# Kernel optimization log

Measured on AMD Instinct MI355X. Metric: run time of the kernel, lower is better.

## Reference

```python
import jax, jax.numpy as jnp
import numpy as np


def setup_inputs() -> dict:
    key = jax.random.key(0)
    k1, k2, k3, k4 = jax.random.split(key, 4)
    B, C, H, W = 4, 48, 512, 512
    T, ws = 3, 64
    # factor matrices (per TensorMultiplication_einsum, T summation terms)
    # init scale: 1/(init_temperature**(1/3) * sqrt(out_dim)) with init_temperature=1.0
    Ws = jax.random.normal(k2, (T, ws, ws), jnp.float32) / np.sqrt(ws)
    Hs = jax.random.normal(k3, (T, ws, ws), jnp.float32) / np.sqrt(ws)
    Cs = jax.random.normal(k4, (T, C, C), jnp.float32) / np.sqrt(C)
    x = jax.random.normal(k1, (B, C, H, W), jnp.float32)
    return {"x": x, "Ws": Ws, "Hs": Hs, "Cs": Cs, "window_size": ws}


def reference(x, Ws, Hs, Cs, window_size):
    """FeatureProcessingBlock forward:
      window_partition -> sum_t einsum('bchw,wW,hH,cC->bCHW') -> window_reverse.
    The window partition/reverse reshapes are fused into one einsum over the
    blocked view (p,q index the window grid; h,w index within-window pixels).
    """
    B, C, H, W = x.shape
    ws = window_size
    # (B, C, H//ws, ws, W//ws, ws)
    xb = x.reshape(B, C, H // ws, ws, W // ws, ws)
    # sum over T terms and contract w, h, c axes with their factor matrices
    out = jnp.einsum('bcphqw,twW,thH,tcC->bCpHqW', xb, Ws, Hs, Cs)
    return out.reshape(B, C, H, W)
```

## Files before the change

### kernel.cpp

```cpp
#include <hip/hip_runtime.h>
#include <hip/hip_bf16.h>


typedef __attribute__((ext_vector_type(8))) short short8;
typedef __attribute__((ext_vector_type(4))) short short4v;
typedef __attribute__((ext_vector_type(4))) float float4v;

#define SMEM_BYTES 97280

static __device__ __forceinline__ unsigned short f2bf(float f) {
  return __builtin_bit_cast(unsigned short, __float2bfloat16(f));
}
static __device__ __forceinline__ unsigned int pk2(float a, float b) {
  return (unsigned int)f2bf(a) | ((unsigned int)f2bf(b) << 16);
}

__global__ __launch_bounds__(512, 2)
void fpb3(const float* __restrict__ x, const float* __restrict__ Ws,
          const float* __restrict__ Hsm, const float* __restrict__ Cs,
          float* __restrict__ out) {
  extern __shared__ char smem[];
  unsigned short* Y1 = (unsigned short*)smem;
  char*           Zb = smem + 27648;
  unsigned short* Cf = (unsigned short*)(smem + 60416);

  int wid = (blockIdx.x & 7) * 128 + (blockIdx.x >> 3);
  int window = wid >> 2, tile = wid & 3;
  int b = window >> 6, p = (window >> 3) & 7, q = window & 7;
  int j0 = tile * 16;

  int tid = threadIdx.x, lane = tid & 63, wave = tid >> 6;
  int lq = lane >> 4, lc = lane & 15;
  int mt = wave & 3, cp = wave >> 2;
  int jg = (lc >> 2) & 1;

  for (int idx = wave; idx < 36; idx += 8) {
    int ss = idx / 3, m = idx - 3 * (idx / 3);
    short8 v;
    #pragma unroll
    for (int e = 0; e < 8; ++e) {
      int k = 8 * lq + e;
      unsigned short u = 0;
      if (k < 12) {
        int cl = k / 3, t = k - 3 * cl;
        u = f2bf(Cs[t * 2304 + (4 * ss + cl) * 48 + 16 * m + lc]);
      }
      v[e] = (short)u;
    }
    *(short8*)&Cf[((ss * 3 + m) * 64 + lane) * 8] = v;
  }
  {
    int px0 = tid, px1 = tid + 512;
    *(unsigned long long*)(Zb + px0 * 32 + ((1 ^ ((px0 >> 2) & 1)) << 4) + 8) = 0ull;
    *(unsigned long long*)(Zb + px1 * 32 + ((1 ^ ((px1 >> 2) & 1)) << 4) + 8) = 0ull;
  }

  short8 wsf[3][2], hsf[3][2];
  #pragma unroll
  for (int t = 0; t < 3; ++t)
    #pragma unroll
    for (int sv = 0; sv < 2; ++sv) {
      short8 aa, bb;
      #pragma unroll
      for (int e = 0; e < 8; ++e) {
        int k = 32 * sv + 8 * lq + e;
        aa[e] = (short)f2bf(Ws [t * 4096 + k * 64 + j0 + lc]);
        bb[e] = (short)f2bf(Hsm[t * 4096 + k * 64 + 16 * mt + lc]);
      }
      wsf[t][sv] = aa; hsf[t][sv] = bb;
    }

  float4v acc[3][8];
  #pragma unroll
  for (int m = 0; m < 3; ++m)
    #pragma unroll
    for (int i = 0; i < 8; ++i) acc[m][i] = float4v{0.f, 0.f, 0.f, 0.f};

  const float* xwin = x + (((size_t)b * 48) * 512 + p * 64) * 512 + q * 64;
  int mA0 = wave >> 2, mA1 = mA0 + 2, cAl = wave & 3;
  const float* sA0 = xwin + ((size_t)(16 * mA0 + lc)) * 512 + 8 * lq;
  const float* sA1 = xwin + ((size_t)(16 * mA1 + lc)) * 512 + 8 * lq;

  float4v fin[8];
  {
    size_t co = (size_t)cAl * 262144;
    fin[0] = *(const float4v*)(sA0 + co);      fin[1] = *(const float4v*)(sA0 + co + 4);
    fin[2] = *(const float4v*)(sA0 + co + 32); fin[3] = *(const float4v*)(sA0 + co + 36);
    fin[4] = *(const float4v*)(sA1 + co);      fin[5] = *(const float4v*)(sA1 + co + 4);
    fin[6] = *(const float4v*)(sA1 + co + 32); fin[7] = *(const float4v*)(sA1 + co + 36);
  }

  __syncthreads();

  for (int s = 0; s < 12; ++s) {
    #pragma unroll
    for (int rep = 0; rep < 2; ++rep) {
      short8 a0, a1;
      #pragma unroll
      for (int e2 = 0; e2 < 4; ++e2) {
        a0[e2]     = (short)f2bf(fin[4 * rep + 0][e2]);
        a0[4 + e2] = (short)f2bf(fin[4 * rep + 1][e2]);
        a1[e2]     = (short)f2bf(fin[4 * rep + 2][e2]);
        a1[4 + e2] = (short)f2bf(fin[4 * rep + 3][e2]);
      }
      int mA = (rep == 0) ? mA0 : mA1;
      #pragma unroll
      for (int t = 0; t < 3; ++t) {
        float4v d = {0.f, 0.f, 0.f, 0.f};
        d = __builtin_amdgcn_mfma_f32_16x16x32_bf16(a0, wsf[t][0], d, 0, 0, 0);
        d = __builtin_amdgcn_mfma_f32_16x16x32_bf16(a1, wsf[t][1], d, 0, 0, 0);
        short4v pv;
        pv[0] = (short)f2bf(d[0]); pv[1] = (short)f2bf(d[1]);
        pv[2] = (short)f2bf(d[2]); pv[3] = (short)f2bf(d[3]);
        *(short4v*)&Y1[(t * 4 + cAl) * 1152 + lc * 72 + 16 * mA + 4 * lq] = pv;
      }
    }
    if (s < 11) {
      size_t co = (size_t)(4 * s + 4 + cAl) * 262144;
      fin[0] = *(const float4v*)(sA0 + co);      fin[1] = *(const float4v*)(sA0 + co + 4);
      fin[2] = *(const float4v*)(sA0 + co + 32); fin[3] = *(const float4v*)(sA0 + co + 36);
      fin[4] = *(const float4v*)(sA1 + co);      fin[5] = *(const float4v*)(sA1 + co + 4);
      fin[6] = *(const float4v*)(sA1 + co + 32); fin[7] = *(const float4v*)(sA1 + co + 36);
    }
    __syncthreads();

    {
      float4v d[3][2];
      #pragma unroll
      for (int t = 0; t < 3; ++t)
        #pragma unroll
        for (int cj = 0; cj < 2; ++cj) {
          const unsigned short* ys = &Y1[(t * 4 + 2 * cp + cj) * 1152 + lc * 72 + 8 * lq];
          short8 y0 = *(const short8*)(ys);
          short8 y1 = *(const short8*)(ys + 32);
          float4v dd = {0.f, 0.f, 0.f, 0.f};
          dd = __builtin_amdgcn_mfma_f32_16x16x32_bf16(hsf[t][0], y0, dd, 0, 0, 0);
          dd = __builtin_amdgcn_mfma_f32_16x16x32_bf16(hsf[t][1], y1, dd, 0, 0, 0);
          d[t][cj] = dd;
        }
      #pragma unroll
      for (int r = 0; r < 4; ++r) {
        int px = (16 * mt + 4 * lq + r) * 16 + lc;
        char* row = Zb + px * 32;
        unsigned int w0 = pk2(d[0][0][r], d[1][0][r]);
        unsigned int w1 = pk2(d[2][0][r], d[0][1][r]);
        unsigned int w2 = pk2(d[1][1][r], d[2][1][r]);
        if (cp == 0) {
          char* g0 = row + ((0 ^ jg) << 4);
          *(unsigned long long*)g0 =
              (unsigned long long)w0 | ((unsigned long long)w1 << 32);
          *(unsigned int*)(g0 + 8) = w2;
        } else {
          *(unsigned int*)(row + ((0 ^ jg) << 4) + 12) = w0;
          char* g1 = row + ((1 ^ jg) << 4);
          *(unsigned long long*)g1 =
              (unsigned long long)w1 | ((unsigned long long)w2 << 32);
        }
      }
    }
    __syncthreads();

    {
      short8 cf0 = *(const short8*)&Cf[((s * 3 + 0) * 64 + lane) * 8];
      short8 cf1 = *(const short8*)&Cf[((s * 3 + 1) * 64 + lane) * 8];
      short8 cf2 = *(const short8*)&Cf[((s * 3 + 2) * 64 + lane) * 8];
      #pragma unroll
      for (int i = 0; i < 8; ++i) {
        int px = 16 * (wave + 8 * i) + lc;
        short8 zf = *(const short8*)(Zb + px * 32 + (((lq & 1) ^ jg) << 4));
        acc[0][i] = __builtin_amdgcn_mfma_f32_16x16x32_bf16(cf0, zf, acc[0][i], 0, 0, 0);
        acc[1][i] = __builtin_amdgcn_mfma_f32_16x16x32_bf16(cf1, zf, acc[1][i], 0, 0, 0);
        acc[2][i] = __builtin_amdgcn_mfma_f32_16x16x32_bf16(cf2, zf, acc[2][i], 0, 0, 0);
      }
    }
  }

  #pragma unroll
  for (int m = 0; m < 3; ++m)
    #pragma unroll
    for (int i = 0; i < 8; ++i) {
      int n = wave + 8 * i;
      size_t rowbase = (((size_t)(b * 48 + 16 * m + 4 * lq)) * 512 + p * 64 + n) * 512
                       + q * 64 + j0 + lc;
      #pragma unroll
      for (int r = 0; r < 4; ++r)
        out[rowbase + (size_t)r * 262144] = acc[m][i][r];
    }
}

extern "C" void kernel_launch(void* const* d_in, const int* in_sizes, int n_in,
                              void* d_out, int out_size, void* d_ws, size_t ws_size,
                              hipStream_t stream) {
  (void)in_sizes; (void)n_in; (void)d_ws; (void)ws_size; (void)out_size;
  const float* x   = (const float*)d_in[0];
  const float* Ws  = (const float*)d_in[1];
  const float* Hsm = (const float*)d_in[2];
  const float* Cs  = (const float*)d_in[3];
  float* out = (float*)d_out;
  (void)hipFuncSetAttribute((const void*)fpb3,
                            hipFuncAttributeMaxDynamicSharedMemorySize, SMEM_BYTES);
  fpb3<<<dim3(1024), dim3(512), SMEM_BYTES, stream>>>(x, Ws, Hsm, Cs, out);
}
```

Before: 176.3 us.

## Process eight channels per stage to halve barriers and channel-mix MFMAs

Processes eight input channels per outer iteration instead of four, so there are six stages instead of twelve. The packed intermediate layout changes to a 48-byte pixel row with three t-groups, which fills 24 of the 32 K slots in the channel-mixing MFMA. This halves the number of syncthreads and of channel-contraction MFMAs. In exchange it uses more LDS for the larger Y1/Z buffers and doubles the register-held x prefetch, which adds register pressure.

```diff
diff --git a/kernel.cpp b/kernel.cpp
--- a/kernel.cpp
+++ b/kernel.cpp
@@ -6,23 +6,26 @@
 typedef __attribute__((ext_vector_type(4))) short short4v;
 typedef __attribute__((ext_vector_type(4))) float float4v;
 
-#define SMEM_BYTES 97280
+#define SMEM_BYTES 118288
 
 static __device__ __forceinline__ unsigned short f2bf(float f) {
   return __builtin_bit_cast(unsigned short, __float2bfloat16(f));
 }
-static __device__ __forceinline__ unsigned int pk2(float a, float b) {
-  return (unsigned int)f2bf(a) | ((unsigned int)f2bf(b) << 16);
+static __device__ __forceinline__ unsigned long long pk4(float a, float b, float c, float d) {
+  unsigned long long lo = (unsigned int)((unsigned int)f2bf(a) | ((unsigned int)f2bf(b) << 16));
+  unsigned long long hi = (unsigned int)((unsigned int)f2bf(c) | ((unsigned int)f2bf(d) << 16));
+  return lo | (hi << 32);
 }
 
 __global__ __launch_bounds__(512, 2)
-void fpb3(const float* __restrict__ x, const float* __restrict__ Ws,
+void fpb4(const float* __restrict__ x, const float* __restrict__ Ws,
           const float* __restrict__ Hsm, const float* __restrict__ Cs,
           float* __restrict__ out) {
   extern __shared__ char smem[];
   unsigned short* Y1 = (unsigned short*)smem;
-  char*           Zb = smem + 27648;
-  unsigned short* Cf = (unsigned short*)(smem + 60416);
+  char* Zb  = smem + 55296;
+  char* Cf  = smem + 104448;
+  char* z16 = smem + 118272;
 
   int wid = (blockIdx.x & 7) * 128 + (blockIdx.x >> 3);
   int window = wid >> 2, tile = wid & 3;
@@ -32,27 +35,18 @@
   int tid = threadIdx.x, lane = tid & 63, wave = tid >> 6;
   int lq = lane >> 4, lc = lane & 15;
   int mt = wave & 3, cp = wave >> 2;
-  int jg = (lc >> 2) & 1;
-
-  for (int idx = wave; idx < 36; idx += 8) {
-    int ss = idx / 3, m = idx - 3 * (idx / 3);
-    short8 v;
-    #pragma unroll
-    for (int e = 0; e < 8; ++e) {
-      int k = 8 * lq + e;
-      unsigned short u = 0;
-      if (k < 12) {
-        int cl = k / 3, t = k - 3 * cl;
-        u = f2bf(Cs[t * 2304 + (4 * ss + cl) * 48 + 16 * m + lc]);
-      }
-      v[e] = (short)u;
-    }
-    *(short8*)&Cf[((ss * 3 + m) * 64 + lane) * 8] = v;
-  }
-  {
-    int px0 = tid, px1 = tid + 512;
-    *(unsigned long long*)(Zb + px0 * 32 + ((1 ^ ((px0 >> 2) & 1)) << 4) + 8) = 0ull;
-    *(unsigned long long*)(Zb + px1 * 32 + ((1 ^ ((px1 >> 2) & 1)) << 4) + 8) = 0ull;
+
+  if (tid < 4) ((unsigned int*)z16)[tid] = 0;
+
+  for (int idx = wave; idx < 18; idx += 8) {
+    int ss = idx / 3, m = idx - 3 * ss;
+    if (lq < 3) {
+      short8 v;
+      #pragma unroll
+      for (int e = 0; e < 8; ++e)
+        v[e] = (short)f2bf(Cs[lq * 2304 + (8 * ss + e) * 48 + 16 * m + lc]);
+      *(short8*)(Cf + (idx * 16 + lc) * 48 + lq * 16) = v;
+    }
   }
 
   short8 wsf[3][2], hsf[3][2];
@@ -76,101 +70,104 @@
     #pragma unroll
     for (int i = 0; i < 8; ++i) acc[m][i] = float4v{0.f, 0.f, 0.f, 0.f};
 
-  const float* xwin = x + (((size_t)b * 48) * 512 + p * 64) * 512 + q * 64;
-  int mA0 = wave >> 2, mA1 = mA0 + 2, cAl = wave & 3;
-  const float* sA0 = xwin + ((size_t)(16 * mA0 + lc)) * 512 + 8 * lq;
-  const float* sA1 = xwin + ((size_t)(16 * mA1 + lc)) * 512 + 8 * lq;
-
-  float4v fin[8];
-  {
-    size_t co = (size_t)cAl * 262144;
-    fin[0] = *(const float4v*)(sA0 + co);      fin[1] = *(const float4v*)(sA0 + co + 4);
-    fin[2] = *(const float4v*)(sA0 + co + 32); fin[3] = *(const float4v*)(sA0 + co + 36);
-    fin[4] = *(const float4v*)(sA1 + co);      fin[5] = *(const float4v*)(sA1 + co + 4);
-    fin[6] = *(const float4v*)(sA1 + co + 32); fin[7] = *(const float4v*)(sA1 + co + 36);
+  const float* xbase = x + (((size_t)b * 48) * 512 + p * 64) * 512 + q * 64
+                         + (size_t)wave * 262144 + (size_t)lc * 512 + 8 * lq;
+
+  float4v fin[2][8];
+  #pragma unroll
+  for (int h = 0; h < 2; ++h) {
+    const float* src = xbase + (size_t)(32 * h) * 512;
+    #pragma unroll
+    for (int j2 = 0; j2 < 2; ++j2) {
+      const float* r = src + (size_t)(16 * j2) * 512;
+      fin[h][4*j2+0] = *(const float4v*)(r);
+      fin[h][4*j2+1] = *(const float4v*)(r + 4);
+      fin[h][4*j2+2] = *(const float4v*)(r + 32);
+      fin[h][4*j2+3] = *(const float4v*)(r + 36);
+    }
   }
 
-  __syncthreads();
-
-  for (int s = 0; s < 12; ++s) {
-    #pragma unroll
-    for (int rep = 0; rep < 2; ++rep) {
-      short8 a0, a1;
-      #pragma unroll
-      for (int e2 = 0; e2 < 4; ++e2) {
-        a0[e2]     = (short)f2bf(fin[4 * rep + 0][e2]);
-        a0[4 + e2] = (short)f2bf(fin[4 * rep + 1][e2]);
-        a1[e2]     = (short)f2bf(fin[4 * rep + 2][e2]);
-        a1[4 + e2] = (short)f2bf(fin[4 * rep + 3][e2]);
-      }
-      int mA = (rep == 0) ? mA0 : mA1;
-      #pragma unroll
-      for (int t = 0; t < 3; ++t) {
-        float4v d = {0.f, 0.f, 0.f, 0.f};
-        d = __builtin_amdgcn_mfma_f32_16x16x32_bf16(a0, wsf[t][0], d, 0, 0, 0);
-        d = __builtin_amdgcn_mfma_f32_16x16x32_bf16(a1, wsf[t][1], d, 0, 0, 0);
-        short4v pv;
-        pv[0] = (short)f2bf(d[0]); pv[1] = (short)f2bf(d[1]);
-        pv[2] = (short)f2bf(d[2]); pv[3] = (short)f2bf(d[3]);
-        *(short4v*)&Y1[(t * 4 + cAl) * 1152 + lc * 72 + 16 * mA + 4 * lq] = pv;
-      }
-    }
-    if (s < 11) {
-      size_t co = (size_t)(4 * s + 4 + cAl) * 262144;
-      fin[0] = *(const float4v*)(sA0 + co);      fin[1] = *(const float4v*)(sA0 + co + 4);
-      fin[2] = *(const float4v*)(sA0 + co + 32); fin[3] = *(const float4v*)(sA0 + co + 36);
-      fin[4] = *(const float4v*)(sA1 + co);      fin[5] = *(const float4v*)(sA1 + co + 4);
-      fin[6] = *(const float4v*)(sA1 + co + 32); fin[7] = *(const float4v*)(sA1 + co + 36);
+  for (int s = 0; s < 6; ++s) {
+    #pragma unroll
+    for (int h = 0; h < 2; ++h) {
+      short8 af[4];
+      #pragma unroll
+      for (int j2 = 0; j2 < 2; ++j2) {
+        short8 a0, a1;
+        #pragma unroll
+        for (int e2 = 0; e2 < 4; ++e2) {
+          a0[e2]   = (short)f2bf(fin[h][4*j2+0][e2]);
+          a0[4+e2] = (short)f2bf(fin[h][4*j2+1][e2]);
+          a1[e2]   = (short)f2bf(fin[h][4*j2+2][e2]);
+          a1[4+e2] = (short)f2bf(fin[h][4*j2+3][e2]);
+        }
+        af[2*j2] = a0; af[2*j2+1] = a1;
+      }
+      if (s < 5) {
+        const float* src = xbase + (size_t)(s + 1) * 2097152 + (size_t)(32 * h) * 512;
+        #pragma unroll
+        for (int j2 = 0; j2 < 2; ++j2) {
+          const float* r = src + (size_t)(16 * j2) * 512;
+          fin[h][4*j2+0] = *(const float4v*)(r);
+          fin[h][4*j2+1] = *(const float4v*)(r + 4);
+          fin[h][4*j2+2] = *(const float4v*)(r + 32);
+          fin[h][4*j2+3] = *(const float4v*)(r + 36);
+        }
+      }
+      #pragma unroll
+      for (int j2 = 0; j2 < 2; ++j2) {
+        int mA = 2 * h + j2;
+        #pragma unroll
+        for (int t = 0; t < 3; ++t) {
+          float4v d = {0.f, 0.f, 0.f, 0.f};
+          d = __builtin_amdgcn_mfma_f32_16x16x32_bf16(af[2*j2],   wsf[t][0], d, 0, 0, 0);
+          d = __builtin_amdgcn_mfma_f32_16x16x32_bf16(af[2*j2+1], wsf[t][1], d, 0, 0, 0);
+          short4v pv;
+          pv[0] = (short)f2bf(d[0]); pv[1] = (short)f2bf(d[1]);
+          pv[2] = (short)f2bf(d[2]); pv[3] = (short)f2bf(d[3]);
+          *(short4v*)&Y1[(t * 8 + wave) * 1152 + lc * 72 + 16 * mA + 4 * lq] = pv;
+        }
+      }
     }
     __syncthreads();
 
-    {
-      float4v d[3][2];
-      #pragma unroll
-      for (int t = 0; t < 3; ++t)
-        #pragma unroll
-        for (int cj = 0; cj < 2; ++cj) {
-          const unsigned short* ys = &Y1[(t * 4 + 2 * cp + cj) * 1152 + lc * 72 + 8 * lq];
-          short8 y0 = *(const short8*)(ys);
-          short8 y1 = *(const short8*)(ys + 32);
-          float4v dd = {0.f, 0.f, 0.f, 0.f};
-          dd = __builtin_amdgcn_mfma_f32_16x16x32_bf16(hsf[t][0], y0, dd, 0, 0, 0);
-          dd = __builtin_amdgcn_mfma_f32_16x16x32_bf16(hsf[t][1], y1, dd, 0, 0, 0);
-          d[t][cj] = dd;
-        }
+    #pragma unroll
+    for (int t = 0; t < 3; ++t) {
+      float4v dB[4];
+      #pragma unroll
+      for (int cj = 0; cj < 4; ++cj) {
+        const unsigned short* ys = &Y1[(t * 8 + 4 * cp + cj) * 1152 + lc * 72 + 8 * lq];
+        short8 y0 = *(const short8*)ys;
+        short8 y1 = *(const short8*)(ys + 32);
+        float4v dd = {0.f, 0.f, 0.f, 0.f};
+        dd = __builtin_amdgcn_mfma_f32_16x16x32_bf16(hsf[t][0], y0, dd, 0, 0, 0);
+        dd = __builtin_amdgcn_mfma_f32_16x16x32_bf16(hsf[t][1], y1, dd, 0, 0, 0);
+        dB[cj] = dd;
+      }
       #pragma unroll
       for (int r = 0; r < 4; ++r) {
         int px = (16 * mt + 4 * lq + r) * 16 + lc;
-        char* row = Zb + px * 32;
-        unsigned int w0 = pk2(d[0][0][r], d[1][0][r]);
-        unsigned int w1 = pk2(d[2][0][r], d[0][1][r]);
-        unsigned int w2 = pk2(d[1][1][r], d[2][1][r]);
-        if (cp == 0) {
-          char* g0 = row + ((0 ^ jg) << 4);
-          *(unsigned long long*)g0 =
-              (unsigned long long)w0 | ((unsigned long long)w1 << 32);
-          *(unsigned int*)(g0 + 8) = w2;
-        } else {
-          *(unsigned int*)(row + ((0 ^ jg) << 4) + 12) = w0;
-          char* g1 = row + ((1 ^ jg) << 4);
-          *(unsigned long long*)g1 =
-              (unsigned long long)w1 | ((unsigned long long)w2 << 32);
-        }
+        *(unsigned long long*)(Zb + px * 48 + 16 * t + 8 * cp) =
+            pk4(dB[0][r], dB[1][r], dB[2][r], dB[3][r]);
       }
     }
     __syncthreads();
 
     {
-      short8 cf0 = *(const short8*)&Cf[((s * 3 + 0) * 64 + lane) * 8];
-      short8 cf1 = *(const short8*)&Cf[((s * 3 + 1) * 64 + lane) * 8];
-      short8 cf2 = *(const short8*)&Cf[((s * 3 + 2) * 64 + lane) * 8];
+      short8 cf[3];
+      #pragma unroll
+      for (int m = 0; m < 3; ++m) {
+        const char* csrc = (lq < 3) ? (Cf + ((s * 3 + m) * 16 + lc) * 48 + lq * 16) : z16;
+        cf[m] = *(const short8*)csrc;
+      }
       #pragma unroll
       for (int i = 0; i < 8; ++i) {
         int px = 16 * (wave + 8 * i) + lc;
-        short8 zf = *(const short8*)(Zb + px * 32 + (((lq & 1) ^ jg) << 4));
-        acc[0][i] = __builtin_amdgcn_mfma_f32_16x16x32_bf16(cf0, zf, acc[0][i], 0, 0, 0);
-        acc[1][i] = __builtin_amdgcn_mfma_f32_16x16x32_bf16(cf1, zf, acc[1][i], 0, 0, 0);
-        acc[2][i] = __builtin_amdgcn_mfma_f32_16x16x32_bf16(cf2, zf, acc[2][i], 0, 0, 0);
+        const char* zsrc = (lq < 3) ? (Zb + px * 48 + 16 * lq) : z16;
+        short8 zf = *(const short8*)zsrc;
+        acc[0][i] = __builtin_amdgcn_mfma_f32_16x16x32_bf16(cf[0], zf, acc[0][i], 0, 0, 0);
+        acc[1][i] = __builtin_amdgcn_mfma_f32_16x16x32_bf16(cf[1], zf, acc[1][i], 0, 0, 0);
+        acc[2][i] = __builtin_amdgcn_mfma_f32_16x16x32_bf16(cf[2], zf, acc[2][i], 0, 0, 0);
       }
     }
   }
@@ -197,7 +194,7 @@
   const float* Hsm = (const float*)d_in[2];
   const float* Cs  = (const float*)d_in[3];
   float* out = (float*)d_out;
-  (void)hipFuncSetAttribute((const void*)fpb3,
+  (void)hipFuncSetAttribute((const void*)fpb4,
                             hipFuncAttributeMaxDynamicSharedMemorySize, SMEM_BYTES);
-  fpb3<<<dim3(1024), dim3(512), SMEM_BYTES, stream>>>(x, Ws, Hsm, Cs, out);
-}
+  fpb4<<<dim3(1024), dim3(512), SMEM_BYTES, stream>>>(x, Ws, Hsm, Cs, out);
+}
```

Result: faster. 162.0 us (-8.1%).
